# Kernel optimization log

Measured on AMD Instinct MI355X. Metric: run time of the kernel, lower is better.

## Reference

```python
import jax, jax.numpy as jnp
import numpy as np

N = 50000        # nodes
E = 800000       # edges
F_IN = 64
HID = [128, 256, 256]
G = 512          # graphs in batch
C = 6            # classes
EPS = 1e-5


def setup_inputs() -> dict:
    key = jax.random.key(0)
    ks = jax.random.split(key, 32)
    inp = {}
    inp['x'] = jax.random.normal(ks[0], (N, F_IN), dtype=jnp.float32)
    inp['edge_index'] = jax.random.randint(ks[1], (2, E), 0, N, dtype=jnp.int64)
    inp['batch'] = jnp.sort(jax.random.randint(ks[2], (N,), 0, G, dtype=jnp.int64))
    dims = [F_IN] + HID
    i = 3
    for l in range(3):
        d_in, d_out = dims[l], dims[l + 1]
        inp[f'W{l+1}'] = jax.random.normal(ks[i], (d_in, d_out), dtype=jnp.float32) * (1.0 / np.sqrt(d_in)); i += 1
        inp[f'b{l+1}'] = jnp.zeros((d_out,), dtype=jnp.float32)
        inp[f'g{l+1}'] = jnp.ones((d_out,), dtype=jnp.float32)
        inp[f'be{l+1}'] = jnp.zeros((d_out,), dtype=jnp.float32)
        inp[f'm{l+1}'] = jax.random.normal(ks[i], (d_out,), dtype=jnp.float32) * 0.1; i += 1
        inp[f'v{l+1}'] = jax.random.uniform(ks[i], (d_out,), dtype=jnp.float32, minval=0.5, maxval=1.5); i += 1
    mlp_dims = [(2 * HID[-1], 256), (256, 128), (128, C)]
    for l, (d_in, d_out) in enumerate(mlp_dims):
        inp[f'Wm{l+1}'] = jax.random.normal(ks[i], (d_in, d_out), dtype=jnp.float32) * (1.0 / np.sqrt(d_in)); i += 1
        inp[f'bm{l+1}'] = jnp.zeros((d_out,), dtype=jnp.float32)
    return inp


def _forward(x, edge_index, batch,
             W1, b1, g1, be1, m1, v1,
             W2, b2, g2, be2, m2, v2,
             W3, b3, g3, be3, m3, v3,
             Wm1, bm1, Wm2, bm2, Wm3, bm3):
    src, dst = edge_index[0], edge_index[1]
    loops = jnp.arange(N, dtype=src.dtype)
    src_sl = jnp.concatenate([src, loops])   # self-loops, as in PyG GCNConv
    dst_sl = jnp.concatenate([dst, loops])
    deg = jax.ops.segment_sum(jnp.ones_like(src_sl, dtype=x.dtype), dst_sl, num_segments=N)
    dis = jnp.where(deg > 0, jax.lax.rsqrt(deg), 0.0)
    norm = dis[src_sl] * dis[dst_sl]          # [E+N]

    def gcn(h, W, b):
        h = h @ W                              # transform first (PyG order)
        msg = h[src_sl] * norm[:, None]        # gather + scale
        return jax.ops.segment_sum(msg, dst_sl, num_segments=N) + b

    def bn_relu(h, g, be, m, v):
        return jax.nn.relu((h - m) * jax.lax.rsqrt(v + EPS) * g + be)

    h = bn_relu(gcn(x, W1, b1), g1, be1, m1, v1)
    h = bn_relu(gcn(h, W2, b2), g2, be2, m2, v2)
    h = bn_relu(gcn(h, W3, b3), g3, be3, m3, v3)

    counts = jax.ops.segment_sum(jnp.ones((N,), dtype=h.dtype), batch, num_segments=G)
    x_mean = jax.ops.segment_sum(h, batch, num_segments=G) / jnp.maximum(counts, 1.0)[:, None]
    x_max = jax.ops.segment_max(h, batch, num_segments=G)
    x_max = jnp.where(counts[:, None] > 0, x_max, 0.0)
    z = jnp.concatenate([x_mean, x_max], axis=1)   # [G, 512]

    z = jax.nn.gelu(z @ Wm1 + bm1, approximate=False)
    z = jax.nn.gelu(z @ Wm2 + bm2, approximate=False)
    return z @ Wm3 + bm3                            # [G, C]


def reference(x, edge_index, batch,
              W1, b1, g1, be1, m1, v1,
              W2, b2, g2, be2, m2, v2,
              W3, b3, g3, be3, m3, v3,
              Wm1, bm1, Wm2, bm2, Wm3, bm3):
    return _forward(x, edge_index, batch,
                    W1, b1, g1, be1, m1, v1,
                    W2, b2, g2, be2, m2, v2,
                    W3, b3, g3, be3, m3, v3,
                    Wm1, bm1, Wm2, bm2, Wm3, bm3)
```

## Files before the change

kernel.cpp:

```cpp
#include <hip/hip_runtime.h>
#include <hip/hip_bf16.h>
#include <hip/hip_fp16.h>

typedef __hip_bfloat16 bf16;
typedef unsigned short u16;
typedef short bfrag __attribute__((ext_vector_type(8)));
typedef float f32x4 __attribute__((ext_vector_type(4)));
typedef unsigned u32x2 __attribute__((ext_vector_type(2)));

#define NGRAPH 512
#define BN_EPS 1e-5f
#define NBUCK 64

__device__ __forceinline__ float b2f(bf16 x) { return __bfloat162float(x); }
__device__ __forceinline__ float bf_lo(unsigned u) { return __uint_as_float(u << 16); }
__device__ __forceinline__ float bf_hi(unsigned u) { return __uint_as_float(u & 0xffff0000u); }
__device__ __forceinline__ u16 f2u(float v) {
    bf16 t = __float2bfloat16(v);
    u16 r; __builtin_memcpy(&r, &t, 2); return r;
}

__device__ __forceinline__ float load_f(const void* p, int i, int isbf16) {
    if (isbf16) {
        unsigned short u = ((const unsigned short*)p)[i];
        return __uint_as_float(((unsigned int)u) << 16);
    }
    return ((const float*)p)[i];
}

__device__ __forceinline__ void repack_sec(const void* W, u16* out, int Kd, int Nd,
                                           int t, int isbf) {
    if (t >= Kd * Nd) return;
    int j = t & 7;
    int lane = (t >> 3) & 63;
    int tile = t >> 9;
    int NT = Nd / 16;
    int nt = tile % NT, kt = tile / NT;
    int k = kt * 32 + (lane >> 4) * 8 + j;
    int nn = nt * 16 + (lane & 15);
    out[t] = f2u(load_f(W, k * Nd + nn, isbf));
}

__device__ __forceinline__ void fold_one(const void* b, const void* g, const void* be,
                                         const void* m, const void* v,
                                         float* S, float* T, int f, int isbf) {
    float bb = load_f(b, f, isbf), gg = load_f(g, f, isbf);
    float bee = load_f(be, f, isbf), mm = load_f(m, f, isbf);
    float vv = load_f(v, f, isbf);
    float s = gg * rsqrtf(vv + BN_EPS);
    S[f] = s;
    T[f] = (bb - mm) * s + bee;
}

__global__ void prep_all(
    const void* __restrict__ x,
    const void* W1, const void* W2, const void* W3,
    const void* b1, const void* g1, const void* be1, const void* m1, const void* v1,
    const void* b2, const void* g2, const void* be2, const void* m2, const void* v2,
    const void* b3, const void* g3, const void* be3, const void* m3, const void* v3,
    u16* __restrict__ xs, u16* W1r, u16* W2r, u16* W3r,
    float* S1, float* T1, float* S2, float* T2, float* S3, float* T3,
    int n, int npad, int* __restrict__ flag) {
    __shared__ int lflag;
    if (threadIdx.x < 64) {
        unsigned short u = ((const unsigned short*)x)[2 * threadIdx.x];
        float f = __uint_as_float(((unsigned int)u) << 16);
        int crazy = (!(fabsf(f) <= 1024.0f)) ? 1 : 0;
        unsigned long long m = __ballot(crazy);
        if (threadIdx.x == 0) lflag = (m == 0ULL) ? 1 : 0;
    }
    __syncthreads();
    const int isbf = lflag;
    const int bid = blockIdx.x;
    const int tid = threadIdx.x;
    if (bid == 0 && tid == 0) *flag = isbf;

    const int nb_cvt = (n * 64 + 255) / 256;
    if (bid < nb_cvt) {
        int i = bid * 256 + tid;
        if (i < n * 64) {
            int node = i >> 6, f = i & 63;
            xs[((size_t)(f >> 5) * npad + node) * 32 + (f & 31)] = f2u(load_f(x, i, isbf));
        }
        return;
    }
    int b2_ = bid - nb_cvt;
    if (b2_ < 32)  { repack_sec(W1, W1r, 64, 128, b2_ * 256 + tid, isbf); return; }
    b2_ -= 32;
    if (b2_ < 128) { repack_sec(W2, W2r, 128, 256, b2_ * 256 + tid, isbf); return; }
    b2_ -= 128;
    if (b2_ < 256) { repack_sec(W3, W3r, 256, 256, b2_ * 256 + tid, isbf); return; }
    b2_ -= 256;
    {
        int t = b2_ * 256 + tid;
        if (t < 128) fold_one(b1, g1, be1, m1, v1, S1, T1, t, isbf);
        else if (t < 384) fold_one(b2, g2, be2, m2, v2, S2, T2, t - 128, isbf);
        else if (t < 640) fold_one(b3, g3, be3, m3, v3, S3, T3, t - 384, isbf);
    }
}

__global__ void init_all(int* __restrict__ deg, int* __restrict__ total,
                         int* __restrict__ bcnt, float* __restrict__ psum,
                         float* __restrict__ pmax, int* __restrict__ pcnt, int n) {
    int i = blockIdx.x * blockDim.x + threadIdx.x;
    if (i < n) deg[i] = 0;
    if (i < NGRAPH * 256) { psum[i] = 0.f; pmax[i] = 0.f; }
    if (i < NGRAPH) pcnt[i] = 0;
    if (i < NBUCK) bcnt[i] = 0;
    if (i == 0) *total = 0;
}

__global__ void count_deg_i(const int* __restrict__ dst, int* __restrict__ deg, int e) {
    int i = blockIdx.x * blockDim.x + threadIdx.x;
    if (i < e) atomicAdd(&deg[dst[i]], 1);
}

__global__ void reserve_rows(const int* __restrict__ deg, int* __restrict__ row_start,
                             int* __restrict__ cursor, float* __restrict__ dis,
                             unsigned* __restrict__ csrw,
                             int* __restrict__ total, int* __restrict__ bcnt, int n) {
    __shared__ int lh[NBUCK];
    int tid = threadIdx.x;
    if (tid < NBUCK) lh[tid] = 0;
    __syncthreads();
    int i = blockIdx.x * blockDim.x + tid;
    if (i < n) {
        int d = deg[i];
        int dpad = (d + 7) & ~7;
        int s = atomicAdd(total, dpad);
        row_start[i] = s;
        cursor[i] = s;
        dis[i] = rsqrtf((float)(d + 1));
        atomicAdd(&lh[min(d, NBUCK - 1)], 1);
        unsigned val = (unsigned)(i & 0xffff);
        for (int k = d; k < dpad; k++) csrw[s + k] = val;
    }
    __syncthreads();
    if (tid < NBUCK) {
        int c = lh[tid];
        if (c) atomicAdd(&bcnt[tid], c);
    }
}

__global__ void bucket_prefix(const int* __restrict__ bcnt, int* __restrict__ bcur) {
    if (threadIdx.x == 0 && blockIdx.x == 0) {
        int acc = 0;
        for (int i = 0; i < NBUCK; i++) { bcur[i] = acc; acc += bcnt[i]; }
    }
}

__global__ void bucket_scatter(const int* __restrict__ deg, const int* __restrict__ rowst,
                               int* __restrict__ bcur, uint4* __restrict__ ninfo, int n) {
    __shared__ int lh[NBUCK];
    __shared__ int lbase[NBUCK];
    int tid = threadIdx.x;
    if (tid < NBUCK) lh[tid] = 0;
    __syncthreads();
    int i = blockIdx.x * blockDim.x + tid;
    int b = 0, lr = 0;
    if (i < n) {
        b = min(deg[i], NBUCK - 1);
        lr = atomicAdd(&lh[b], 1);
    }
    __syncthreads();
    if (tid < NBUCK) {
        int c = lh[tid];
        lbase[tid] = c ? atomicAdd(&bcur[tid], c) : 0;
    }
    __syncthreads();
    if (i < n) ninfo[lbase[b] + lr] = make_uint4(i, rowst[i], deg[i], 0);
}

__global__ void scatter_edges(const int* __restrict__ src, const int* __restrict__ dst,
                              const float* __restrict__ dis, int* __restrict__ cursor,
                              unsigned* __restrict__ csrw, int e) {
    int i = blockIdx.x * blockDim.x + threadIdx.x;
    if (i >= e) return;
    int s = src[i], dt = dst[i];
    int pos = atomicAdd(&cursor[dt], 1);
    float nw = dis[s] * dis[dt];
    unsigned short h = __half_as_ushort(__float2half(nw));
    csrw[pos] = (unsigned)(s & 0xffff) | ((unsigned)h << 16);
}

template <int NSLICE>
__global__ __launch_bounds__(256) void csr_agg_s5(
    const uint4* __restrict__ ninfo, const unsigned* __restrict__ csrw,
    const u16* __restrict__ hs, u16* __restrict__ AG, int n, int npad) {
    constexpr int F = NSLICE * 32;
    int slice = blockIdx.x % NSLICE;
    int nb = blockIdx.x / NSLICE;
    int lane = threadIdx.x & 63;
    int wv = threadIdx.x >> 6;
    int sub = lane >> 3, ls = lane & 7;
    int oidx = nb * 32 + wv * 8 + sub;
    if (oidx >= n) return;
    uint4 nf = ninfo[oidx];
    int node = (int)nf.x;
    int start = (int)nf.y;
    int d = (int)nf.z;
    int dpad = (d + 7) & ~7;
    float dd = 1.0f / (float)(d + 1);
    const u16* __restrict__ base = hs + (size_t)slice * npad * 32;

    float a0, a1, a2, a3;
    {
        uint2 u = *(const uint2*)(base + (size_t)node * 32 + ls * 4);
        a0 = bf_lo(u.x) * dd; a1 = bf_hi(u.x) * dd;
        a2 = bf_lo(u.y) * dd; a3 = bf_hi(u.y) * dd;
    }

    const unsigned* __restrict__ ep = csrw + start;
    unsigned mc[8];
    if (dpad) {
#pragma unroll
        for (int j = 0; j < 8; j++) mc[j] = ep[j];
    }
    for (int k = 0; k < dpad; k += 8) {
        unsigned mn[8];
        if (k + 8 < dpad) {
#pragma unroll
            for (int j = 0; j < 8; j++) mn[j] = ep[k + 8 + j];
        }
        float w[8];
        uint2 q[8];
#pragma unroll
        for (int j = 0; j < 8; j++) {
            int s = (int)(mc[j] & 0xffffu);
            w[j] = __half2float(__ushort_as_half((unsigned short)(mc[j] >> 16)));
            q[j] = *(const uint2*)(base + (size_t)s * 32 + ls * 4);
        }
#pragma unroll
        for (int j = 0; j < 8; j++) {
            a0 += w[j] * bf_lo(q[j].x); a1 += w[j] * bf_hi(q[j].x);
            a2 += w[j] * bf_lo(q[j].y); a3 += w[j] * bf_hi(q[j].y);
        }
#pragma unroll
        for (int j = 0; j < 8; j++) mc[j] = mn[j];
    }
    u32x2 o;
    o.x = (unsigned)f2u(a0) | ((unsigned)f2u(a1) << 16);
    o.y = (unsigned)f2u(a2) | ((unsigned)f2u(a3) << 16);
    __builtin_nontemporal_store(o, (u32x2*)(AG + (size_t)node * F + slice * 32 + ls * 4));
}

template <int K, int N, int NSUB, int NSLICE_OUT>
__global__ __launch_bounds__(256) void mfma_gemm_dg(
    const u16* __restrict__ A, const u16* __restrict__ Wrep,
    const float* __restrict__ S, const float* __restrict__ T,
    u16* __restrict__ C, int M, int npad, int ntiles) {
    constexpr int NT = N / 16;
    constexpr int KT = K / 32;
    constexpr int NSPLIT = NT / NSUB;
    int bid = blockIdx.x;
    int g = bid >> 3;
    int ns = g % NSPLIT;
    int mt = (bid & 7) + 8 * (g / NSPLIT);
    if (mt >= ntiles) return;
    const int tid = threadIdx.x;
    const int lane = tid & 63;
    const int wv = tid >> 6;
    const int mrow = lane & 15;
    const int kb = lane >> 4;

    bfrag breg[KT * NSUB];
#pragma unroll
    for (int kt = 0; kt < KT; kt++)
#pragma unroll
        for (int j = 0; j < NSUB; j++)
            breg[kt * NSUB + j] = *(const bfrag*)(Wrep +
                ((size_t)(kt * NT + ns * NSUB + j) * 64 + lane) * 8);

    const u16* __restrict__ arow = A + (size_t)(mt * 64 + wv * 16 + mrow) * K + kb * 8;
    bfrag areg[KT];
#pragma unroll
    for (int kt = 0; kt < KT; kt++)
        areg[kt] = *(const bfrag*)(arow + kt * 32);

    f32x4 acc[NSUB];
#pragma unroll
    for (int j = 0; j < NSUB; j++) acc[j] = (f32x4){0.f, 0.f, 0.f, 0.f};
#pragma unroll
    for (int kt = 0; kt < KT; kt++)
#pragma unroll
        for (int j = 0; j < NSUB; j++)
            acc[j] = __builtin_amdgcn_mfma_f32_16x16x32_bf16(areg[kt], breg[kt * NSUB + j], acc[j], 0, 0, 0);

    const int m0 = mt * 64;
#pragma unroll
    for (int j = 0; j < NSUB; j++) {
        int f = (ns * NSUB + j) * 16 + mrow;
        float s = S[f];
        float t = T[f];
#pragma unroll
        for (int r = 0; r < 4; r++) {
            int row = m0 + wv * 16 + kb * 4 + r;
            if (row < M) {
                u16 val = f2u(fmaxf(acc[j][r] * s + t, 0.0f));
                if (NSLICE_OUT > 0)
                    C[((size_t)(f >> 5) * npad + row) * 32 + (f & 31)] = val;
                else
                    C[(size_t)row * N + f] = val;
            }
        }
    }
}

#define POOL_NC 64
__global__ __launch_bounds__(256) void pool_seg(
    const u16* __restrict__ h, const int* __restrict__ batch,
    float* __restrict__ psum, float* __restrict__ pmax,
    int* __restrict__ pcnt, int n) {
    int wid = (int)(((size_t)blockIdx.x * blockDim.x + threadIdx.x) >> 6);
    int lane = threadIdx.x & 63;
    int n0 = wid * POOL_NC;
    if (n0 >= n) return;
    int n1 = min(n0 + POOL_NC, n);

    float sum[4] = {0.f, 0.f, 0.f, 0.f};
    float mx[4] = {0.f, 0.f, 0.f, 0.f};
    int cnt = 0;
    int gcur = batch[n0];

    uint2 u_next = *(const uint2*)(h + (size_t)n0 * 256 + lane * 4);
    int g_next = gcur;

    for (int node = n0; node < n1; node++) {
        uint2 u = u_next;
        int g = g_next;
        if (node + 1 < n1) {
            u_next = *(const uint2*)(h + (size_t)(node + 1) * 256 + lane * 4);
            g_next = batch[node + 1];
        }
        if (g != gcur) {
#pragma unroll
            for (int c = 0; c < 4; c++) {
                atomicAdd(&psum[gcur * 256 + lane * 4 + c], sum[c]);
                atomicMax((int*)&pmax[gcur * 256 + lane * 4 + c], __float_as_int(mx[c]));
                sum[c] = 0.f; mx[c] = 0.f;
            }
            if (lane == 0) atomicAdd(&pcnt[gcur], cnt);
            cnt = 0;
            gcur = g;
        }
        float v0 = bf_lo(u.x), v1 = bf_hi(u.x), v2 = bf_lo(u.y), v3 = bf_hi(u.y);
        sum[0] += v0; sum[1] += v1; sum[2] += v2; sum[3] += v3;
        mx[0] = fmaxf(mx[0], v0); mx[1] = fmaxf(mx[1], v1);
        mx[2] = fmaxf(mx[2], v2); mx[3] = fmaxf(mx[3], v3);
        cnt++;
    }
#pragma unroll
    for (int c = 0; c < 4; c++) {
        atomicAdd(&psum[gcur * 256 + lane * 4 + c], sum[c]);
        atomicMax((int*)&pmax[gcur * 256 + lane * 4 + c], __float_as_int(mx[c]));
    }
    if (lane == 0) atomicAdd(&pcnt[gcur], cnt);
}

__global__ void mlp_gemm1(const float* __restrict__ psum, const float* __restrict__ pmax,
                          const int* __restrict__ pcnt, const void* __restrict__ W,
                          const void* __restrict__ bias, float* __restrict__ C,
                          const int* __restrict__ flag) {
    __shared__ float a[512];
    int row = blockIdx.x;
    float invc = 1.0f / (float)max(pcnt[row], 1);
    int idx = threadIdx.x;
    a[idx] = psum[row * 256 + idx] * invc;
    a[256 + idx] = pmax[row * 256 + idx];
    __syncthreads();
    int col = threadIdx.x;
    int isbf = *flag;
    float acc = load_f(bias, col, isbf);
    if (isbf) {
        const bf16* w = (const bf16*)W;
        for (int k = 0; k < 512; k++) acc += a[k] * b2f(w[k * 256 + col]);
    } else {
        const float* w = (const float*)W;
        for (int k = 0; k < 512; k++) acc += a[k] * w[k * 256 + col];
    }
    acc = 0.5f * acc * (1.0f + erff(acc * 0.70710678118654752f));
    C[row * 256 + col] = acc;
}

template <int K, int NOUT, bool GELU>
__global__ void mlp_gemm(const float* __restrict__ A, const void* __restrict__ W,
                         const void* __restrict__ bias, float* __restrict__ C,
                         const int* __restrict__ flag) {
    __shared__ float a[K];
    int row = blockIdx.x;
    for (int idx = threadIdx.x; idx < K; idx += blockDim.x) a[idx] = A[row * K + idx];
    __syncthreads();
    int col = threadIdx.x;
    if (col < NOUT) {
        int isbf = *flag;
        float acc = load_f(bias, col, isbf);
        if (isbf) {
            const bf16* w = (const bf16*)W;
            for (int k = 0; k < K; k++) acc += a[k] * b2f(w[k * NOUT + col]);
        } else {
            const float* w = (const float*)W;
            for (int k = 0; k < K; k++) acc += a[k] * w[k * NOUT + col];
        }
        if (GELU) acc = 0.5f * acc * (1.0f + erff(acc * 0.70710678118654752f));
        C[row * NOUT + col] = acc;
    }
}

__global__ void mlp_gemm3(const float* __restrict__ A, const void* __restrict__ W,
                          const void* __restrict__ bias, void* __restrict__ out,
                          const int* __restrict__ flag) {
    __shared__ float a[128];
    int row = blockIdx.x;
    if (threadIdx.x < 128) a[threadIdx.x] = A[row * 128 + threadIdx.x];
    __syncthreads();
    int col = threadIdx.x;
    if (col < 6) {
        int isbf = *flag;
        float acc = load_f(bias, col, isbf);
        if (isbf) {
            const bf16* w = (const bf16*)W;
            for (int k = 0; k < 128; k++) acc += a[k] * b2f(w[k * 6 + col]);
        } else {
            const float* w = (const float*)W;
            for (int k = 0; k < 128; k++) acc += a[k] * w[k * 6 + col];
        }
        if (isbf) ((bf16*)out)[row * 6 + col] = __float2bfloat16(acc);
        else      ((float*)out)[row * 6 + col] = acc;
    }
}

extern "C" void kernel_launch(void* const* d_in, const int* in_sizes, int n_in,
                              void* d_out, int out_size, void* d_ws, size_t ws_size,
                              hipStream_t stream) {
    const void* x     = d_in[0];
    const int*  ei    = (const int*)d_in[1];
    const int*  batch = (const int*)d_in[2];
    const void *W1 = d_in[3],  *b1 = d_in[4],  *g1 = d_in[5],  *be1 = d_in[6],  *m1 = d_in[7],  *v1 = d_in[8];
    const void *W2 = d_in[9],  *b2 = d_in[10], *g2 = d_in[11], *be2 = d_in[12], *m2 = d_in[13], *v2 = d_in[14];
    const void *W3 = d_in[15], *b3 = d_in[16], *g3 = d_in[17], *be3 = d_in[18], *m3 = d_in[19], *v3 = d_in[20];
    const void *Wm1 = d_in[21], *bm1 = d_in[22];
    const void *Wm2 = d_in[23], *bm2 = d_in[24];
    const void *Wm3 = d_in[25], *bm3 = d_in[26];

    const int n = in_sizes[0] / 64;
    const int E = in_sizes[1] / 2;
    const int* src = ei;
    const int* dst = ei + E;
    const int npad = (n + 63 + 64) & ~63;
    const int ntiles = (n + 63) / 64;
    const int ntp8 = (ntiles + 7) & ~7;

    size_t off = 0;
    auto carve = [&](size_t bytes) {
        void* p = (char*)d_ws + off;
        off += (bytes + 255) & ~(size_t)255;
        return p;
    };
    int*      flag  = (int*)carve(4);
    int*      total = (int*)carve(4);
    int*      bcnt  = (int*)carve(NBUCK * 4);
    int*      bcur  = (int*)carve(NBUCK * 4);
    float*    dis   = (float*)carve((size_t)n * 4);
    int*      deg_i = (int*)carve((size_t)n * 4);
    int*      rowst = (int*)carve((size_t)n * 4);
    int*      curs  = (int*)carve((size_t)n * 4);
    uint4*    ninfo = (uint4*)carve((size_t)n * 16);
    unsigned* csrw  = (unsigned*)carve(((size_t)E + 8 * (size_t)n) * 4);
    u16*      xs    = (u16*)carve((size_t)npad * 64 * 2);
    u16*      Hs    = (u16*)carve((size_t)npad * 256 * 2);
    u16*      AG    = (u16*)carve((size_t)npad * 256 * 2);
    u16*      H     = (u16*)carve((size_t)npad * 256 * 2);
    u16*      W1r   = (u16*)carve((size_t)64 * 128 * 2);
    u16*      W2r   = (u16*)carve((size_t)128 * 256 * 2);
    u16*      W3r   = (u16*)carve((size_t)256 * 256 * 2);
    float* S1 = (float*)carve(128 * 4); float* T1 = (float*)carve(128 * 4);
    float* S2 = (float*)carve(256 * 4); float* T2 = (float*)carve(256 * 4);
    float* S3 = (float*)carve(256 * 4); float* T3 = (float*)carve(256 * 4);
    float* psum = (float*)carve((size_t)NGRAPH * 256 * 4);
    float* pmax = (float*)carve((size_t)NGRAPH * 256 * 4);
    int*   pcnt = (int*)carve((size_t)NGRAPH * 4);
    float* z1   = (float*)carve((size_t)NGRAPH * 256 * 4);
    float* z2   = (float*)carve((size_t)NGRAPH * 128 * 4);
    (void)ws_size; (void)n_in;

    const int BT = 256;

    const int nb_cvt = (n * 64 + 255) / 256;
    prep_all<<<nb_cvt + 32 + 128 + 256 + 3, BT, 0, stream>>>(
        x, W1, W2, W3,
        b1, g1, be1, m1, v1, b2, g2, be2, m2, v2, b3, g3, be3, m3, v3,
        xs, W1r, W2r, W3r, S1, T1, S2, T2, S3, T3, n, npad, flag);

    init_all<<<(NGRAPH * 256 + BT - 1) / BT, BT, 0, stream>>>(deg_i, total, bcnt, psum, pmax, pcnt, n);
    count_deg_i<<<(E + BT - 1) / BT, BT, 0, stream>>>(dst, deg_i, E);
    reserve_rows<<<(n + BT - 1) / BT, BT, 0, stream>>>(deg_i, rowst, curs, dis, csrw, total, bcnt, n);
    bucket_prefix<<<1, 64, 0, stream>>>(bcnt, bcur);
    bucket_scatter<<<(n + BT - 1) / BT, BT, 0, stream>>>(deg_i, rowst, bcur, ninfo, n);
    scatter_edges<<<(E + BT - 1) / BT, BT, 0, stream>>>(src, dst, dis, curs, csrw, E);

    const int nb32 = (n + 31) / 32;

    csr_agg_s5<2><<<2 * nb32, 256, 0, stream>>>(ninfo, csrw, xs, AG, n, npad);
    mfma_gemm_dg<64, 128, 4, 4><<<2 * ntp8, 256, 0, stream>>>(AG, W1r, S1, T1, Hs, n, npad, ntiles);

    csr_agg_s5<4><<<4 * nb32, 256, 0, stream>>>(ninfo, csrw, Hs, AG, n, npad);
    mfma_gemm_dg<128, 256, 4, 8><<<4 * ntp8, 256, 0, stream>>>(AG, W2r, S2, T2, Hs, n, npad, ntiles);

    csr_agg_s5<8><<<8 * nb32, 256, 0, stream>>>(ninfo, csrw, Hs, AG, n, npad);
    mfma_gemm_dg<256, 256, 2, 0><<<8 * ntp8, 256, 0, stream>>>(AG, W3r, S3, T3, H, n, npad, ntiles);

    const int pool_waves = (n + POOL_NC - 1) / POOL_NC;
    pool_seg<<<(pool_waves * 64 + BT - 1) / BT, BT, 0, stream>>>(H, batch, psum, pmax, pcnt, n);
    mlp_gemm1<<<NGRAPH, 256, 0, stream>>>(psum, pmax, pcnt, Wm1, bm1, z1, flag);
    mlp_gemm<256, 128, true><<<NGRAPH, 256, 0, stream>>>(z1, Wm2, bm2, z2, flag);
    mlp_gemm3<<<NGRAPH, 128, 0, stream>>>(z2, Wm3, bm3, d_out, flag);
}
```

Baseline: 445.8 us.

## Merge init into prep, fuse bucket prefix/scatter with edge scatter, fuse MLP

The workspace-zeroing kernel becomes extra blocks of the prep kernel. The bucket prefix, bucket scatter and edge scatter are merged into one launch, with each block recomputing the 64-bucket prefix locally and claiming slots through a separate counter. The three MLP kernels become one kernel per graph that keeps intermediates in shared memory. Together this drops five launches and the z1/z2 global round trips, but the fused MLP runs its smaller layers with only part of the block active.

```diff
diff --git a/kernel.cpp b/kernel.cpp
--- a/kernel.cpp
+++ b/kernel.cpp
@@ -60,6 +60,9 @@
     const void* b3, const void* g3, const void* be3, const void* m3, const void* v3,
     u16* __restrict__ xs, u16* W1r, u16* W2r, u16* W3r,
     float* S1, float* T1, float* S2, float* T2, float* S3, float* T3,
+    int* __restrict__ deg, int* __restrict__ total, int* __restrict__ bcnt,
+    int* __restrict__ claim, float* __restrict__ psum, float* __restrict__ pmax,
+    int* __restrict__ pcnt,
     int n, int npad, int* __restrict__ flag) {
     __shared__ int lflag;
     if (threadIdx.x < 64) {
@@ -91,23 +94,22 @@
     b2_ -= 128;
     if (b2_ < 256) { repack_sec(W3, W3r, 256, 256, b2_ * 256 + tid, isbf); return; }
     b2_ -= 256;
-    {
+    if (b2_ < 3) {
         int t = b2_ * 256 + tid;
         if (t < 128) fold_one(b1, g1, be1, m1, v1, S1, T1, t, isbf);
         else if (t < 384) fold_one(b2, g2, be2, m2, v2, S2, T2, t - 128, isbf);
         else if (t < 640) fold_one(b3, g3, be3, m3, v3, S3, T3, t - 384, isbf);
-    }
-}
-
-__global__ void init_all(int* __restrict__ deg, int* __restrict__ total,
-                         int* __restrict__ bcnt, float* __restrict__ psum,
-                         float* __restrict__ pmax, int* __restrict__ pcnt, int n) {
-    int i = blockIdx.x * blockDim.x + threadIdx.x;
-    if (i < n) deg[i] = 0;
-    if (i < NGRAPH * 256) { psum[i] = 0.f; pmax[i] = 0.f; }
-    if (i < NGRAPH) pcnt[i] = 0;
-    if (i < NBUCK) bcnt[i] = 0;
-    if (i == 0) *total = 0;
+        return;
+    }
+    b2_ -= 3;
+    {
+        int i = b2_ * 256 + tid;
+        if (i < n) deg[i] = 0;
+        if (i < NGRAPH * 256) { psum[i] = 0.f; pmax[i] = 0.f; }
+        if (i < NGRAPH) pcnt[i] = 0;
+        if (i < NBUCK) { bcnt[i] = 0; claim[i] = 0; }
+        if (i == 0) *total = 0;
+    }
 }
 
 __global__ void count_deg_i(const int* __restrict__ dst, int* __restrict__ deg, int e) {
@@ -142,21 +144,34 @@
     }
 }
 
-__global__ void bucket_prefix(const int* __restrict__ bcnt, int* __restrict__ bcur) {
-    if (threadIdx.x == 0 && blockIdx.x == 0) {
-        int acc = 0;
-        for (int i = 0; i < NBUCK; i++) { bcur[i] = acc; acc += bcnt[i]; }
-    }
-}
-
-__global__ void bucket_scatter(const int* __restrict__ deg, const int* __restrict__ rowst,
-                               int* __restrict__ bcur, uint4* __restrict__ ninfo, int n) {
+__global__ void scatter_all(const int* __restrict__ src, const int* __restrict__ dst,
+                            const float* __restrict__ dis, int* __restrict__ cursor,
+                            unsigned* __restrict__ csrw,
+                            const int* __restrict__ deg, const int* __restrict__ rowst,
+                            const int* __restrict__ bcnt, int* __restrict__ claim,
+                            uint4* __restrict__ ninfo, int e, int n, int nbE) {
+    int bid = blockIdx.x;
+    int tid = threadIdx.x;
+    if (bid < nbE) {
+        int i = bid * 256 + tid;
+        if (i >= e) return;
+        int s = src[i], dt = dst[i];
+        int pos = atomicAdd(&cursor[dt], 1);
+        float nw = dis[s] * dis[dt];
+        unsigned short h = __half_as_ushort(__float2half(nw));
+        csrw[pos] = (unsigned)(s & 0xffff) | ((unsigned)h << 16);
+        return;
+    }
     __shared__ int lh[NBUCK];
     __shared__ int lbase[NBUCK];
-    int tid = threadIdx.x;
+    __shared__ int lpre[NBUCK];
     if (tid < NBUCK) lh[tid] = 0;
-    __syncthreads();
-    int i = blockIdx.x * blockDim.x + tid;
+    if (tid == 0) {
+        int acc = 0;
+        for (int k = 0; k < NBUCK; k++) { lpre[k] = acc; acc += bcnt[k]; }
+    }
+    __syncthreads();
+    int i = (bid - nbE) * 256 + tid;
     int b = 0, lr = 0;
     if (i < n) {
         b = min(deg[i], NBUCK - 1);
@@ -165,22 +180,10 @@
     __syncthreads();
     if (tid < NBUCK) {
         int c = lh[tid];
-        lbase[tid] = c ? atomicAdd(&bcur[tid], c) : 0;
+        lbase[tid] = c ? (lpre[tid] + atomicAdd(&claim[tid], c)) : 0;
     }
     __syncthreads();
     if (i < n) ninfo[lbase[b] + lr] = make_uint4(i, rowst[i], deg[i], 0);
-}
-
-__global__ void scatter_edges(const int* __restrict__ src, const int* __restrict__ dst,
-                              const float* __restrict__ dis, int* __restrict__ cursor,
-                              unsigned* __restrict__ csrw, int e) {
-    int i = blockIdx.x * blockDim.x + threadIdx.x;
-    if (i >= e) return;
-    int s = src[i], dt = dst[i];
-    int pos = atomicAdd(&cursor[dt], 1);
-    float nw = dis[s] * dis[dt];
-    unsigned short h = __half_as_ushort(__float2half(nw));
-    csrw[pos] = (unsigned)(s & 0xffff) | ((unsigned)h << 16);
 }
 
 template <int NSLICE>
@@ -357,75 +360,58 @@
     if (lane == 0) atomicAdd(&pcnt[gcur], cnt);
 }
 
-__global__ void mlp_gemm1(const float* __restrict__ psum, const float* __restrict__ pmax,
-                          const int* __restrict__ pcnt, const void* __restrict__ W,
-                          const void* __restrict__ bias, float* __restrict__ C,
-                          const int* __restrict__ flag) {
+__global__ __launch_bounds__(256) void mlp_fused(
+    const float* __restrict__ psum, const float* __restrict__ pmax,
+    const int* __restrict__ pcnt,
+    const void* __restrict__ Wm1, const void* __restrict__ bm1,
+    const void* __restrict__ Wm2, const void* __restrict__ bm2,
+    const void* __restrict__ Wm3, const void* __restrict__ bm3,
+    void* __restrict__ out, const int* __restrict__ flag) {
     __shared__ float a[512];
+    __shared__ float h1[256];
+    __shared__ float h2[128];
     int row = blockIdx.x;
+    int tid = threadIdx.x;
+    int isbf = *flag;
     float invc = 1.0f / (float)max(pcnt[row], 1);
-    int idx = threadIdx.x;
-    a[idx] = psum[row * 256 + idx] * invc;
-    a[256 + idx] = pmax[row * 256 + idx];
-    __syncthreads();
-    int col = threadIdx.x;
-    int isbf = *flag;
-    float acc = load_f(bias, col, isbf);
-    if (isbf) {
-        const bf16* w = (const bf16*)W;
-        for (int k = 0; k < 512; k++) acc += a[k] * b2f(w[k * 256 + col]);
-    } else {
-        const float* w = (const float*)W;
-        for (int k = 0; k < 512; k++) acc += a[k] * w[k * 256 + col];
-    }
-    acc = 0.5f * acc * (1.0f + erff(acc * 0.70710678118654752f));
-    C[row * 256 + col] = acc;
-}
-
-template <int K, int NOUT, bool GELU>
-__global__ void mlp_gemm(const float* __restrict__ A, const void* __restrict__ W,
-                         const void* __restrict__ bias, float* __restrict__ C,
-                         const int* __restrict__ flag) {
-    __shared__ float a[K];
-    int row = blockIdx.x;
-    for (int idx = threadIdx.x; idx < K; idx += blockDim.x) a[idx] = A[row * K + idx];
-    __syncthreads();
-    int col = threadIdx.x;
-    if (col < NOUT) {
-        int isbf = *flag;
-        float acc = load_f(bias, col, isbf);
+    a[tid] = psum[row * 256 + tid] * invc;
+    a[256 + tid] = pmax[row * 256 + tid];
+    __syncthreads();
+    {
+        float acc = load_f(bm1, tid, isbf);
         if (isbf) {
-            const bf16* w = (const bf16*)W;
-            for (int k = 0; k < K; k++) acc += a[k] * b2f(w[k * NOUT + col]);
+            const bf16* w = (const bf16*)Wm1;
+            for (int k = 0; k < 512; k++) acc += a[k] * b2f(w[k * 256 + tid]);
         } else {
-            const float* w = (const float*)W;
-            for (int k = 0; k < K; k++) acc += a[k] * w[k * NOUT + col];
-        }
-        if (GELU) acc = 0.5f * acc * (1.0f + erff(acc * 0.70710678118654752f));
-        C[row * NOUT + col] = acc;
-    }
-}
-
-__global__ void mlp_gemm3(const float* __restrict__ A, const void* __restrict__ W,
-                          const void* __restrict__ bias, void* __restrict__ out,
-                          const int* __restrict__ flag) {
-    __shared__ float a[128];
-    int row = blockIdx.x;
-    if (threadIdx.x < 128) a[threadIdx.x] = A[row * 128 + threadIdx.x];
-    __syncthreads();
-    int col = threadIdx.x;
-    if (col < 6) {
-        int isbf = *flag;
-        float acc = load_f(bias, col, isbf);
+            const float* w = (const float*)Wm1;
+            for (int k = 0; k < 512; k++) acc += a[k] * w[k * 256 + tid];
+        }
+        h1[tid] = 0.5f * acc * (1.0f + erff(acc * 0.70710678118654752f));
+    }
+    __syncthreads();
+    if (tid < 128) {
+        float acc = load_f(bm2, tid, isbf);
         if (isbf) {
-            const bf16* w = (const bf16*)W;
-            for (int k = 0; k < 128; k++) acc += a[k] * b2f(w[k * 6 + col]);
+            const bf16* w = (const bf16*)Wm2;
+            for (int k = 0; k < 256; k++) acc += h1[k] * b2f(w[k * 128 + tid]);
         } else {
-            const float* w = (const float*)W;
-            for (int k = 0; k < 128; k++) acc += a[k] * w[k * 6 + col];
-        }
-        if (isbf) ((bf16*)out)[row * 6 + col] = __float2bfloat16(acc);
-        else      ((float*)out)[row * 6 + col] = acc;
+            const float* w = (const float*)Wm2;
+            for (int k = 0; k < 256; k++) acc += h1[k] * w[k * 128 + tid];
+        }
+        h2[tid] = 0.5f * acc * (1.0f + erff(acc * 0.70710678118654752f));
+    }
+    __syncthreads();
+    if (tid < 6) {
+        float acc = load_f(bm3, tid, isbf);
+        if (isbf) {
+            const bf16* w = (const bf16*)Wm3;
+            for (int k = 0; k < 128; k++) acc += h2[k] * b2f(w[k * 6 + tid]);
+        } else {
+            const float* w = (const float*)Wm3;
+            for (int k = 0; k < 128; k++) acc += h2[k] * w[k * 6 + tid];
+        }
+        if (isbf) ((bf16*)out)[row * 6 + tid] = __float2bfloat16(acc);
+        else      ((float*)out)[row * 6 + tid] = acc;
     }
 }
 
@@ -459,7 +445,7 @@
     int*      flag  = (int*)carve(4);
     int*      total = (int*)carve(4);
     int*      bcnt  = (int*)carve(NBUCK * 4);
-    int*      bcur  = (int*)carve(NBUCK * 4);
+    int*      claim = (int*)carve(NBUCK * 4);
     float*    dis   = (float*)carve((size_t)n * 4);
     int*      deg_i = (int*)carve((size_t)n * 4);
     int*      rowst = (int*)carve((size_t)n * 4);
@@ -479,24 +465,24 @@
     float* psum = (float*)carve((size_t)NGRAPH * 256 * 4);
     float* pmax = (float*)carve((size_t)NGRAPH * 256 * 4);
     int*   pcnt = (int*)carve((size_t)NGRAPH * 4);
-    float* z1   = (float*)carve((size_t)NGRAPH * 256 * 4);
-    float* z2   = (float*)carve((size_t)NGRAPH * 128 * 4);
     (void)ws_size; (void)n_in;
 
     const int BT = 256;
 
     const int nb_cvt = (n * 64 + 255) / 256;
-    prep_all<<<nb_cvt + 32 + 128 + 256 + 3, BT, 0, stream>>>(
+    const int nb_init = (NGRAPH * 256 + 255) / 256;
+    prep_all<<<nb_cvt + 32 + 128 + 256 + 3 + nb_init, BT, 0, stream>>>(
         x, W1, W2, W3,
         b1, g1, be1, m1, v1, b2, g2, be2, m2, v2, b3, g3, be3, m3, v3,
-        xs, W1r, W2r, W3r, S1, T1, S2, T2, S3, T3, n, npad, flag);
-
-    init_all<<<(NGRAPH * 256 + BT - 1) / BT, BT, 0, stream>>>(deg_i, total, bcnt, psum, pmax, pcnt, n);
+        xs, W1r, W2r, W3r, S1, T1, S2, T2, S3, T3,
+        deg_i, total, bcnt, claim, psum, pmax, pcnt, n, npad, flag);
+
     count_deg_i<<<(E + BT - 1) / BT, BT, 0, stream>>>(dst, deg_i, E);
     reserve_rows<<<(n + BT - 1) / BT, BT, 0, stream>>>(deg_i, rowst, curs, dis, csrw, total, bcnt, n);
-    bucket_prefix<<<1, 64, 0, stream>>>(bcnt, bcur);
-    bucket_scatter<<<(n + BT - 1) / BT, BT, 0, stream>>>(deg_i, rowst, bcur, ninfo, n);
-    scatter_edges<<<(E + BT - 1) / BT, BT, 0, stream>>>(src, dst, dis, curs, csrw, E);
+    const int nbE = (E + BT - 1) / BT;
+    const int nbN = (n + BT - 1) / BT;
+    scatter_all<<<nbE + nbN, BT, 0, stream>>>(src, dst, dis, curs, csrw,
+                                              deg_i, rowst, bcnt, claim, ninfo, E, n, nbE);
 
     const int nb32 = (n + 31) / 32;
 
@@ -511,7 +497,5 @@
 
     const int pool_waves = (n + POOL_NC - 1) / POOL_NC;
     pool_seg<<<(pool_waves * 64 + BT - 1) / BT, BT, 0, stream>>>(H, batch, psum, pmax, pcnt, n);
-    mlp_gemm1<<<NGRAPH, 256, 0, stream>>>(psum, pmax, pcnt, Wm1, bm1, z1, flag);
-    mlp_gemm<256, 128, true><<<NGRAPH, 256, 0, stream>>>(z1, Wm2, bm2, z2, flag);
-    mlp_gemm3<<<NGRAPH, 128, 0, stream>>>(z2, Wm3, bm3, d_out, flag);
-}
+    mlp_fused<<<NGRAPH, 256, 0, stream>>>(psum, pmax, pcnt, Wm1, bm1, Wm2, bm2, Wm3, bm3, d_out, flag);
+}
```

Result: faster. 436.1 us (-2.2%).
